# Kernel optimization log

Hardware: AMD Instinct MI355X
Metric: run time of the kernel (lower is better)

Reference implementation:

```python
import jax, jax.numpy as jnp
import numpy as np

B, S, D = 4, 4096, 2048
DFF = 4 * D
SKIP = 0.125


def setup_inputs() -> dict:
    key = jax.random.key(0)
    ks = jax.random.split(key, 4)
    s_in = 1.0 / np.sqrt(D).astype(np.float32)
    s_ff = 1.0 / np.sqrt(DFF).astype(np.float32)
    return {
        "x": jax.random.normal(ks[0], (B, S, D), jnp.float32),
        "Wr": jax.random.normal(ks[1], (D, 1), jnp.float32) * s_in,
        "br": jnp.zeros((1,), jnp.float32),
        "W1": jax.random.normal(ks[2], (D, DFF), jnp.float32) * s_in,
        "b1": jnp.zeros((DFF,), jnp.float32),
        "W2": jax.random.normal(ks[3], (DFF, D), jnp.float32) * s_ff,
        "b2": jnp.zeros((D,), jnp.float32),
    }


def reference(x, Wr, br, W1, b1, W2, b2):
    Bs, Ss, Ds = x.shape
    k = max(int(Ss * SKIP), 1)
    # Router: tiny linear D -> 1
    logits = (x @ Wr + br)[..., 0]                      # [B, S]
    # Top-k token selection along sequence
    weights, idx = jax.lax.top_k(logits, k)             # [B, k] (unsorted order within topk)
    perm = jnp.argsort(idx, axis=1)                     # torch.sort's sort-indices
    tokens = jnp.take_along_axis(idx, perm, axis=1)     # sorted token positions [B, k]
    # Gather selected tokens
    fx = jnp.take_along_axis(x, tokens[..., None], axis=1)  # [B, k, D]
    h = jax.nn.gelu(fx @ W1 + b1, approximate=False)    # [B, k, 4D]
    out_l = h @ W2 + b2                                  # [B, k, D]
    # Softmax over topk router logits, reordered to sorted-token order
    tw = jax.nn.softmax(weights, axis=1)                # [B, k]
    rw = jnp.take_along_axis(tw, perm, axis=1)          # [B, k]
    xw = rw[..., None] * out_l                           # [B, k, D]
    # scatter_add back onto x at the selected token positions
    bidx = jnp.arange(Bs)[:, None]                       # [B, 1]
    return x.at[bidx, tokens].add(xw)
```

## Files before the change

### kernel.cpp

```cpp
#include <hip/hip_runtime.h>
#include <math.h>

#define B_DIM   4
#define S_DIM   4096
#define D_DIM   2048
#define DFF_DIM 8192
#define K_TOP   512
#define M_ROWS  (B_DIM * K_TOP)
#define NSPLIT  4

typedef _Float16 half8 __attribute__((ext_vector_type(8)));
typedef _Float16 half4 __attribute__((ext_vector_type(4)));
typedef float    floatx4 __attribute__((ext_vector_type(4)));

static const size_t OFF_LOGITS = 0;
static const size_t OFF_SELMAP = 0;
static const size_t OFF_TOK    = 65536;
static const size_t OFF_RW     = 73728;
static const size_t OFF_FX     = 81920;
static const size_t OFF_W1T    = OFF_FX  + (size_t)M_ROWS * D_DIM * 2;
static const size_t OFF_W2T    = OFF_W1T + (size_t)DFF_DIM * D_DIM * 2;
static const size_t OFF_H      = OFF_W2T + (size_t)D_DIM * DFF_DIM * 2;
static const size_t WS_NEEDED  = OFF_H   + (size_t)M_ROWS * DFF_DIM * 2;
static const size_t OFF_PART   = OFF_W1T;

__device__ __forceinline__ void async_ld16(const void* g, void* l) {
  __builtin_amdgcn_global_load_lds((const __attribute__((address_space(1))) unsigned int*)g,
                                   (__attribute__((address_space(3))) unsigned int*)l,
                                   16, 0, 0);
}

#define WAITCNT_VM4   0x0F74
#define WAITCNT_VM0   0x0F70
#define WAITCNT_LGKM0 0xC07F

__global__ __launch_bounds__(256) void router_logits(const float* __restrict__ x,
                                                     const float* __restrict__ Wr,
                                                     const float* __restrict__ br,
                                                     float* __restrict__ logits) {
  int row  = blockIdx.x * 4 + (threadIdx.x >> 6);
  int lane = threadIdx.x & 63;
  const float4* xr = (const float4*)(x + (size_t)row * D_DIM);
  const float4* wr = (const float4*)Wr;
  float s = 0.f;
#pragma unroll
  for (int i = 0; i < (D_DIM / 4) / 64; ++i) {
    float4 a = xr[lane + i * 64];
    float4 w = wr[lane + i * 64];
    s += a.x * w.x + a.y * w.y + a.z * w.z + a.w * w.w;
  }
#pragma unroll
  for (int off = 32; off > 0; off >>= 1) s += __shfl_down(s, off, 64);
  if (lane == 0) logits[row] = s + br[0];
}

__global__ __launch_bounds__(256) void topk_select(const float* logits,
                                                   int* selmap,
                                                   int* __restrict__ tokens,
                                                   float* __restrict__ rw) {
  int b = blockIdx.x;
  const float* lg = logits + (size_t)b * S_DIM;
  __shared__ unsigned int keys[S_DIM];
  __shared__ unsigned int bins[256];
  __shared__ unsigned int sscan[256];
  __shared__ unsigned int sh_prefix, sh_r;
  __shared__ float sel_logit[K_TOP];
  __shared__ float red[8];

  int tid = threadIdx.x;
  for (int s = tid; s < S_DIM; s += 256) {
    unsigned int u = __float_as_uint(lg[s]);
    keys[s] = (u & 0x80000000u) ? ~u : (u | 0x80000000u);
    selmap[b * S_DIM + s] = -1;
  }
  if (tid == 0) { sh_prefix = 0u; sh_r = K_TOP; }
  __syncthreads();

  for (int p = 24; p >= 0; p -= 8) {
    bins[tid] = 0u;
    __syncthreads();
    unsigned int prefix = sh_prefix;
    unsigned int maskhi = (p == 24) ? 0u : (0xFFFFFFFFu << (p + 8));
    for (int s = tid; s < S_DIM; s += 256) {
      unsigned int kk = keys[s];
      if ((kk & maskhi) == prefix) atomicAdd(&bins[(kk >> p) & 255u], 1u);
    }
    __syncthreads();
    sscan[tid] = bins[255 - tid];
    __syncthreads();
#pragma unroll
    for (int off = 1; off < 256; off <<= 1) {
      unsigned int v = (tid >= off) ? sscan[tid - off] : 0u;
      __syncthreads();
      sscan[tid] += v;
      __syncthreads();
    }
    unsigned int r = sh_r;
    unsigned int above = (tid > 0) ? sscan[tid - 1] : 0u;
    bool hit = (sscan[tid] >= r) && (above < r);
    __syncthreads();
    if (hit) {
      sh_prefix = prefix | ((unsigned int)(255 - tid) << p);
      sh_r = r - above;
    }
    __syncthreads();
  }
  unsigned int T = sh_prefix;

  int s0 = tid * 16;
  unsigned int g = 0, e = 0;
#pragma unroll
  for (int j = 0; j < 16; ++j) {
    unsigned int kk = keys[s0 + j];
    g += (kk > T);
    e += (kk == T);
  }
  sscan[tid] = g | (e << 16);
  __syncthreads();
#pragma unroll
  for (int off = 1; off < 256; off <<= 1) {
    unsigned int v = (tid >= off) ? sscan[tid - off] : 0u;
    __syncthreads();
    sscan[tid] += v;
    __syncthreads();
  }
  unsigned int incl = sscan[tid];
  unsigned int Gtot = sscan[255] & 0xFFFFu;
  unsigned int need = (unsigned int)K_TOP - Gtot;
  unsigned int gr = (incl & 0xFFFFu) - g;
  unsigned int er = (incl >> 16) - e;
#pragma unroll
  for (int j = 0; j < 16; ++j) {
    unsigned int kk = keys[s0 + j];
    if (kk > T) {
      unsigned int pos = gr + (er < need ? er : need);
      tokens[b * K_TOP + (int)pos] = s0 + j;
      sel_logit[pos] = __uint_as_float((kk & 0x80000000u) ? (kk & 0x7FFFFFFFu) : ~kk);
      selmap[b * S_DIM + s0 + j] = (int)pos;
      gr++;
    } else if (kk == T) {
      if (er < need) {
        unsigned int pos = gr + er;
        tokens[b * K_TOP + (int)pos] = s0 + j;
        sel_logit[pos] = __uint_as_float((kk & 0x80000000u) ? (kk & 0x7FFFFFFFu) : ~kk);
        selmap[b * S_DIM + s0 + j] = (int)pos;
      }
      er++;
    }
  }
  __syncthreads();

  int lane = tid & 63, wv = tid >> 6;
  float mx = -1e30f;
  for (int i = tid; i < K_TOP; i += 256) mx = fmaxf(mx, sel_logit[i]);
#pragma unroll
  for (int off = 32; off > 0; off >>= 1) mx = fmaxf(mx, __shfl_down(mx, off, 64));
  if (lane == 0) red[wv] = mx;
  __syncthreads();
  if (tid == 0) red[0] = fmaxf(fmaxf(red[0], red[1]), fmaxf(red[2], red[3]));
  __syncthreads();
  float M = red[0];
  float sm = 0.f;
  for (int i = tid; i < K_TOP; i += 256) sm += expf(sel_logit[i] - M);
#pragma unroll
  for (int off = 32; off > 0; off >>= 1) sm += __shfl_down(sm, off, 64);
  if (lane == 0) red[4 + wv] = sm;
  __syncthreads();
  if (tid == 0) red[4] = red[4] + red[5] + red[6] + red[7];
  __syncthreads();
  float SUM = red[4];
  for (int i = tid; i < K_TOP; i += 256) rw[b * K_TOP + i] = expf(sel_logit[i] - M) / SUM;
}

__global__ __launch_bounds__(256) void transpose_cvt(const float* __restrict__ in,
                                                     _Float16* __restrict__ out,
                                                     int K, int N) {
  __shared__ float tile[64][65];
  int nb = blockIdx.x * 64, kb = blockIdx.y * 64;
  int tid = threadIdx.x;
  int lr = tid >> 4;
  int lc = (tid & 15) * 4;
#pragma unroll
  for (int p = 0; p < 4; ++p) {
    int row = p * 16 + lr;
    float4 v = *(const float4*)(in + (size_t)(kb + row) * N + nb + lc);
    tile[row][lc] = v.x; tile[row][lc + 1] = v.y; tile[row][lc + 2] = v.z; tile[row][lc + 3] = v.w;
  }
  __syncthreads();
#pragma unroll
  for (int p = 0; p < 2; ++p) {
    int cc = p * 256 + tid;
    int n  = cc >> 3;
    int kc = (cc & 7) * 8;
    half8 o;
#pragma unroll
    for (int j = 0; j < 8; ++j) o[j] = (_Float16)tile[kc + j][n];
    *(half8*)(out + (size_t)(nb + n) * K + kb + kc) = o;
  }
}

__global__ __launch_bounds__(256) void gather_cvt(const float* __restrict__ x,
                                                  const int* __restrict__ tokens,
                                                  _Float16* __restrict__ fx) {
  int row = blockIdx.x;
  int b = row >> 9;
  int token = tokens[row];
  const float4* src = (const float4*)(x + ((size_t)b * S_DIM + token) * D_DIM);
  half4* dst = (half4*)(fx + (size_t)row * D_DIM);
  for (int i = threadIdx.x; i < D_DIM / 4; i += 256) {
    float4 v = src[i];
    half4 o;
    o[0] = (_Float16)v.x; o[1] = (_Float16)v.y; o[2] = (_Float16)v.z; o[3] = (_Float16)v.w;
    dst[i] = o;
  }
}

template <int EPI>
__global__ __launch_bounds__(256) void gemm_bt(const _Float16* __restrict__ A,
                                               const _Float16* __restrict__ Bt,
                                               const float* __restrict__ bias,
                                               _Float16* __restrict__ Co,
                                               int M, int N, int K, int Kspan) {
  __shared__ _Float16 As[2][128 * 32];
  __shared__ _Float16 Bs[2][128 * 32];
  const int tid = threadIdx.x;
  const int lane = tid & 63;
  const int wave = tid >> 6;
  const int bm = blockIdx.y * 128;
  const int bn = blockIdx.x * 128;
  const int wm = (wave & 1) * 64;
  const int wn = (wave >> 1) * 64;
  const int mr = lane & 15;
  const int sw = ((lane >> 4) ^ ((lane >> 1) & 3)) * 8;
  const int k0 = blockIdx.z * Kspan;
  const int kend = k0 + Kspan;

  const int c0 = (wave * 2) * 64 + lane;
  const int c1 = (wave * 2 + 1) * 64 + lane;
  const int m0 = c0 >> 2, g0 = (c0 & 3) ^ ((m0 >> 1) & 3);
  const int m1 = c1 >> 2, g1 = (c1 & 3) ^ ((m1 >> 1) & 3);
  const _Float16* a0p = A  + (size_t)(bm + m0) * K + g0 * 8;
  const _Float16* a1p = A  + (size_t)(bm + m1) * K + g1 * 8;
  const _Float16* b0p = Bt + (size_t)(bn + m0) * K + g0 * 8;
  const _Float16* b1p = Bt + (size_t)(bn + m1) * K + g1 * 8;
  const int slot0 = (wave * 2) * 512;
  const int slot1 = (wave * 2 + 1) * 512;

  floatx4 acc[4][4] = {};

  async_ld16(a0p + k0, &As[0][slot0]);
  async_ld16(b0p + k0, &Bs[0][slot0]);
  async_ld16(a1p + k0, &As[0][slot1]);
  async_ld16(b1p + k0, &Bs[0][slot1]);

  for (int kt = k0; kt < kend; kt += 64) {
    {
      int kn = kt + 32;
      async_ld16(a0p + kn, &As[1][slot0]);
      async_ld16(b0p + kn, &Bs[1][slot0]);
      async_ld16(a1p + kn, &As[1][slot1]);
      async_ld16(b1p + kn, &Bs[1][slot1]);
      __builtin_amdgcn_s_waitcnt(WAITCNT_VM4);
    }
    __builtin_amdgcn_s_barrier();
    {
      half8 af[4], bf[4];
#pragma unroll
      for (int i = 0; i < 4; ++i) af[i] = *(const half8*)(&As[0][(wm + i * 16 + mr) * 32 + sw]);
#pragma unroll
      for (int j = 0; j < 4; ++j) bf[j] = *(const half8*)(&Bs[0][(wn + j * 16 + mr) * 32 + sw]);
#pragma unroll
      for (int i = 0; i < 4; ++i)
#pragma unroll
        for (int j = 0; j < 4; ++j)
          acc[i][j] = __builtin_amdgcn_mfma_f32_16x16x32_f16(af[i], bf[j], acc[i][j], 0, 0, 0);
    }
    __builtin_amdgcn_s_waitcnt(WAITCNT_LGKM0);
    __builtin_amdgcn_s_barrier();

    if (kt + 64 < kend) {
      int kn = kt + 64;
      async_ld16(a0p + kn, &As[0][slot0]);
      async_ld16(b0p + kn, &Bs[0][slot0]);
      async_ld16(a1p + kn, &As[0][slot1]);
      async_ld16(b1p + kn, &Bs[0][slot1]);
      __builtin_amdgcn_s_waitcnt(WAITCNT_VM4);
    } else {
      __builtin_amdgcn_s_waitcnt(WAITCNT_VM0);
    }
    __builtin_amdgcn_s_barrier();
    {
      half8 af[4], bf[4];
#pragma unroll
      for (int i = 0; i < 4; ++i) af[i] = *(const half8*)(&As[1][(wm + i * 16 + mr) * 32 + sw]);
#pragma unroll
      for (int j = 0; j < 4; ++j) bf[j] = *(const half8*)(&Bs[1][(wn + j * 16 + mr) * 32 + sw]);
#pragma unroll
      for (int i = 0; i < 4; ++i)
#pragma unroll
        for (int j = 0; j < 4; ++j)
          acc[i][j] = __builtin_amdgcn_mfma_f32_16x16x32_f16(af[i], bf[j], acc[i][j], 0, 0, 0);
    }
    __builtin_amdgcn_s_waitcnt(WAITCNT_LGKM0);
    __builtin_amdgcn_s_barrier();
  }

  const int r0 = (lane >> 4) * 4;
  const int cn = lane & 15;
  if (EPI == 0) {
#pragma unroll
    for (int i = 0; i < 4; ++i)
#pragma unroll
      for (int j = 0; j < 4; ++j) {
        int col = bn + wn + j * 16 + cn;
        float bv = bias[col];
#pragma unroll
        for (int r = 0; r < 4; ++r) {
          int row = bm + wm + i * 16 + r0 + r;
          float v = acc[i][j][r] + bv;
          v = 0.5f * v * (1.0f + erff(v * 0.7071067811865475f));
          Co[(size_t)row * N + col] = (_Float16)v;
        }
      }
  } else {
    size_t zoff = (size_t)blockIdx.z * M;
#pragma unroll
    for (int i = 0; i < 4; ++i)
#pragma unroll
      for (int j = 0; j < 4; ++j) {
        int col = bn + wn + j * 16 + cn;
#pragma unroll
        for (int r = 0; r < 4; ++r) {
          int row = bm + wm + i * 16 + r0 + r;
          Co[(zoff + row) * N + col] = (_Float16)acc[i][j][r];
        }
      }
  }
}

__global__ __launch_bounds__(256) void finalize(const float* __restrict__ x,
                                                const _Float16* __restrict__ part,
                                                const float* __restrict__ bias,
                                                const int* __restrict__ selmap,
                                                const float* __restrict__ rw,
                                                float* __restrict__ out) {
  int row = blockIdx.x;
  size_t base = (size_t)row * D_DIM;
  int sel = selmap[row];
  int c = threadIdx.x * 8;
  float4 o0 = *(const float4*)(x + base + c);
  float4 o1 = *(const float4*)(x + base + c + 4);
  if (sel >= 0) {
    float wgt = rw[sel];
    float acc[8] = {0, 0, 0, 0, 0, 0, 0, 0};
#pragma unroll
    for (int kz = 0; kz < NSPLIT; ++kz) {
      half8 p = *(const half8*)(part + ((size_t)kz * M_ROWS + sel) * D_DIM + c);
#pragma unroll
      for (int j = 0; j < 8; ++j) acc[j] += (float)p[j];
    }
    float4 b0 = *(const float4*)(bias + c);
    float4 b1 = *(const float4*)(bias + c + 4);
    o0.x += wgt * (acc[0] + b0.x);
    o0.y += wgt * (acc[1] + b0.y);
    o0.z += wgt * (acc[2] + b0.z);
    o0.w += wgt * (acc[3] + b0.w);
    o1.x += wgt * (acc[4] + b1.x);
    o1.y += wgt * (acc[5] + b1.y);
    o1.z += wgt * (acc[6] + b1.z);
    o1.w += wgt * (acc[7] + b1.w);
  }
  *(float4*)(out + base + c)     = o0;
  *(float4*)(out + base + c + 4) = o1;
}

extern "C" void kernel_launch(void* const* d_in, const int* in_sizes, int n_in,
                              void* d_out, int out_size, void* d_ws, size_t ws_size,
                              hipStream_t stream) {
  const float* x  = (const float*)d_in[0];
  const float* Wr = (const float*)d_in[1];
  const float* br = (const float*)d_in[2];
  const float* W1 = (const float*)d_in[3];
  const float* b1 = (const float*)d_in[4];
  const float* W2 = (const float*)d_in[5];
  const float* b2 = (const float*)d_in[6];
  float* out = (float*)d_out;

  if (ws_size < WS_NEEDED) return;

  char* ws = (char*)d_ws;
  float*     logits = (float*)(ws + OFF_LOGITS);
  int*       selmap = (int*)(ws + OFF_SELMAP);
  int*       tokens = (int*)(ws + OFF_TOK);
  float*     rw     = (float*)(ws + OFF_RW);
  _Float16*  fx     = (_Float16*)(ws + OFF_FX);
  _Float16*  W1T    = (_Float16*)(ws + OFF_W1T);
  _Float16*  W2T    = (_Float16*)(ws + OFF_W2T);
  _Float16*  h      = (_Float16*)(ws + OFF_H);
  _Float16*  part   = (_Float16*)(ws + OFF_PART);

  transpose_cvt<<<dim3(DFF_DIM / 64, D_DIM / 64), 256, 0, stream>>>(W1, W1T, D_DIM, DFF_DIM);
  transpose_cvt<<<dim3(D_DIM / 64, DFF_DIM / 64), 256, 0, stream>>>(W2, W2T, DFF_DIM, D_DIM);

  router_logits<<<(B_DIM * S_DIM) / 4, 256, 0, stream>>>(x, Wr, br, logits);
  topk_select<<<B_DIM, 256, 0, stream>>>(logits, selmap, tokens, rw);
  gather_cvt<<<M_ROWS, 256, 0, stream>>>(x, tokens, fx);

  gemm_bt<0><<<dim3(DFF_DIM / 128, M_ROWS / 128, 1), 256, 0, stream>>>(
      fx, W1T, b1, h, M_ROWS, DFF_DIM, D_DIM, D_DIM);
  gemm_bt<2><<<dim3(D_DIM / 128, M_ROWS / 128, NSPLIT), 256, 0, stream>>>(
      h, W2T, nullptr, part, M_ROWS, D_DIM, DFF_DIM, DFF_DIM / NSPLIT);
  finalize<<<B_DIM * S_DIM, 256, 0, stream>>>(x, part, b2, selmap, rw, out);
}
```

Measured before the change: 600.7 us.

## Replace 128x128 GEMM with 256x256 tile, 8-wave kernel and block swizzle

Both FFN GEMMs move to a new kernel with 256x256 output tiles, 512 threads (8 waves) and 64-wide K tiles in double-buffered LDS. The K loop runs in four MFMA phases with s_setprio around the math, an XOR swizzle on the LDS layout, and a workgroup remap that groups blocks for L2 reuse. The aim is more reuse per loaded byte and more MFMA work per barrier. In exchange the kernel needs 128 KB of LDS per block and many more accumulator registers, and the second GEMM runs fewer blocks (8x8x4), which can limit occupancy.

```diff
diff --git a/kernel.cpp b/kernel.cpp
--- a/kernel.cpp
+++ b/kernel.cpp
@@ -30,7 +30,6 @@
                                    16, 0, 0);
 }
 
-#define WAITCNT_VM4   0x0F74
 #define WAITCNT_VM0   0x0F70
 #define WAITCNT_LGKM0 0xC07F
 
@@ -216,92 +215,135 @@
 }
 
 template <int EPI>
-__global__ __launch_bounds__(256) void gemm_bt(const _Float16* __restrict__ A,
-                                               const _Float16* __restrict__ Bt,
-                                               const float* __restrict__ bias,
-                                               _Float16* __restrict__ Co,
-                                               int M, int N, int K, int Kspan) {
-  __shared__ _Float16 As[2][128 * 32];
-  __shared__ _Float16 Bs[2][128 * 32];
-  const int tid = threadIdx.x;
+__global__ __launch_bounds__(512, 2) void gemm256(const _Float16* __restrict__ A,
+                                                  const _Float16* __restrict__ Bt,
+                                                  const float* __restrict__ bias,
+                                                  _Float16* __restrict__ Co,
+                                                  int M, int N, int K, int Kspan) {
+  __shared__ _Float16 As[2][256 * 64];
+  __shared__ _Float16 Bs[2][256 * 64];
+  const int tid  = threadIdx.x;
   const int lane = tid & 63;
   const int wave = tid >> 6;
-  const int bm = blockIdx.y * 128;
-  const int bn = blockIdx.x * 128;
-  const int wm = (wave & 1) * 64;
-  const int wn = (wave >> 1) * 64;
-  const int mr = lane & 15;
-  const int sw = ((lane >> 4) ^ ((lane >> 1) & 3)) * 8;
+  const int wm   = wave >> 2;
+  const int wn   = wave & 3;
+
+  const int nwg = gridDim.x * gridDim.y;
+  const int bid = blockIdx.y * gridDim.x + blockIdx.x;
+  const int swb = (bid & 7) * (nwg >> 3) + (bid >> 3);
+  const int bn  = (swb % gridDim.x) * 256;
+  const int bm  = (swb / gridDim.x) * 256;
+
   const int k0 = blockIdx.z * Kspan;
-  const int kend = k0 + Kspan;
-
-  const int c0 = (wave * 2) * 64 + lane;
-  const int c1 = (wave * 2 + 1) * 64 + lane;
-  const int m0 = c0 >> 2, g0 = (c0 & 3) ^ ((m0 >> 1) & 3);
-  const int m1 = c1 >> 2, g1 = (c1 & 3) ^ ((m1 >> 1) & 3);
-  const _Float16* a0p = A  + (size_t)(bm + m0) * K + g0 * 8;
-  const _Float16* a1p = A  + (size_t)(bm + m1) * K + g1 * 8;
-  const _Float16* b0p = Bt + (size_t)(bn + m0) * K + g0 * 8;
-  const _Float16* b1p = Bt + (size_t)(bn + m1) * K + g1 * 8;
-  const int slot0 = (wave * 2) * 512;
-  const int slot1 = (wave * 2 + 1) * 512;
-
-  floatx4 acc[4][4] = {};
-
-  async_ld16(a0p + k0, &As[0][slot0]);
-  async_ld16(b0p + k0, &Bs[0][slot0]);
-  async_ld16(a1p + k0, &As[0][slot1]);
-  async_ld16(b1p + k0, &Bs[0][slot1]);
-
-  for (int kt = k0; kt < kend; kt += 64) {
-    {
-      int kn = kt + 32;
-      async_ld16(a0p + kn, &As[1][slot0]);
-      async_ld16(b0p + kn, &Bs[1][slot0]);
-      async_ld16(a1p + kn, &As[1][slot1]);
-      async_ld16(b1p + kn, &Bs[1][slot1]);
-      __builtin_amdgcn_s_waitcnt(WAITCNT_VM4);
-    }
-    __builtin_amdgcn_s_barrier();
-    {
-      half8 af[4], bf[4];
-#pragma unroll
-      for (int i = 0; i < 4; ++i) af[i] = *(const half8*)(&As[0][(wm + i * 16 + mr) * 32 + sw]);
-#pragma unroll
-      for (int j = 0; j < 4; ++j) bf[j] = *(const half8*)(&Bs[0][(wn + j * 16 + mr) * 32 + sw]);
-#pragma unroll
-      for (int i = 0; i < 4; ++i)
-#pragma unroll
-        for (int j = 0; j < 4; ++j)
-          acc[i][j] = __builtin_amdgcn_mfma_f32_16x16x32_f16(af[i], bf[j], acc[i][j], 0, 0, 0);
-    }
+  const int nt = Kspan / 64;
+
+  const int lr  = lane >> 3;
+  const int lcs = ((lane & 7) ^ lr) * 8;
+  const _Float16* sa[2][2];
+  const _Float16* sb[2][2];
+  int ldso[2][2];
+#pragma unroll
+  for (int h = 0; h < 2; ++h)
+#pragma unroll
+    for (int ci = 0; ci < 2; ++ci) {
+      const int cip = 2 * wave + ci;
+      const int r   = h * 128 + cip * 8 + lr;
+      sa[h][ci] = A  + (size_t)(bm + r) * K + k0 + lcs;
+      sb[h][ci] = Bt + (size_t)(bn + r) * K + k0 + lcs;
+      ldso[h][ci] = h * 8192 + cip * 512;
+    }
+
+  const int mr   = lane & 15;
+  const int ksub = lane >> 4;
+  const int xr   = mr & 7;
+  const int sc0  = (ksub ^ xr) * 8;
+  const int sc1  = ((ksub ^ xr) ^ 4) * 8;
+  const int aro  = (wm * 128 + mr) * 64;
+  const int bro  = (wn * 64 + mr) * 64;
+
+  floatx4 acc[8][4] = {};
+
+#pragma unroll
+  for (int h = 0; h < 2; ++h)
+#pragma unroll
+    for (int ci = 0; ci < 2; ++ci) {
+      async_ld16(sa[h][ci], &As[0][ldso[h][ci]]);
+      async_ld16(sb[h][ci], &Bs[0][ldso[h][ci]]);
+    }
+  __builtin_amdgcn_s_waitcnt(WAITCNT_VM0);
+  __builtin_amdgcn_s_barrier();
+
+  for (int t = 0; t < nt; ++t) {
+    const _Float16* as = As[t & 1];
+    const _Float16* bs = Bs[t & 1];
+    half8 af[4], bf[4];
+
+#pragma unroll
+    for (int i = 0; i < 4; ++i) af[i] = *(const half8*)(as + aro + i * 1024 + sc0);
+#pragma unroll
+    for (int j = 0; j < 4; ++j) bf[j] = *(const half8*)(bs + bro + j * 1024 + sc0);
+    if (t + 1 < nt) {
+      const int nb = (t + 1) & 1;
+      const int kt = (t + 1) * 64;
+#pragma unroll
+      for (int h = 0; h < 2; ++h)
+#pragma unroll
+        for (int ci = 0; ci < 2; ++ci) {
+          async_ld16(sa[h][ci] + kt, &As[nb][ldso[h][ci]]);
+          async_ld16(sb[h][ci] + kt, &Bs[nb][ldso[h][ci]]);
+        }
+    }
+    __builtin_amdgcn_s_barrier();
     __builtin_amdgcn_s_waitcnt(WAITCNT_LGKM0);
-    __builtin_amdgcn_s_barrier();
-
-    if (kt + 64 < kend) {
-      int kn = kt + 64;
-      async_ld16(a0p + kn, &As[0][slot0]);
-      async_ld16(b0p + kn, &Bs[0][slot0]);
-      async_ld16(a1p + kn, &As[0][slot1]);
-      async_ld16(b1p + kn, &Bs[0][slot1]);
-      __builtin_amdgcn_s_waitcnt(WAITCNT_VM4);
-    } else {
-      __builtin_amdgcn_s_waitcnt(WAITCNT_VM0);
-    }
-    __builtin_amdgcn_s_barrier();
-    {
-      half8 af[4], bf[4];
-#pragma unroll
-      for (int i = 0; i < 4; ++i) af[i] = *(const half8*)(&As[1][(wm + i * 16 + mr) * 32 + sw]);
-#pragma unroll
-      for (int j = 0; j < 4; ++j) bf[j] = *(const half8*)(&Bs[1][(wn + j * 16 + mr) * 32 + sw]);
-#pragma unroll
-      for (int i = 0; i < 4; ++i)
-#pragma unroll
-        for (int j = 0; j < 4; ++j)
-          acc[i][j] = __builtin_amdgcn_mfma_f32_16x16x32_f16(af[i], bf[j], acc[i][j], 0, 0, 0);
-    }
+    __builtin_amdgcn_s_setprio(1);
+#pragma unroll
+    for (int i = 0; i < 4; ++i)
+#pragma unroll
+      for (int j = 0; j < 4; ++j)
+        acc[i][j] = __builtin_amdgcn_mfma_f32_16x16x32_f16(af[i], bf[j], acc[i][j], 0, 0, 0);
+    __builtin_amdgcn_s_setprio(0);
+    __builtin_amdgcn_s_barrier();
+
+#pragma unroll
+    for (int i = 0; i < 4; ++i) af[i] = *(const half8*)(as + aro + 4096 + i * 1024 + sc0);
+    __builtin_amdgcn_s_barrier();
     __builtin_amdgcn_s_waitcnt(WAITCNT_LGKM0);
+    __builtin_amdgcn_s_setprio(1);
+#pragma unroll
+    for (int i = 0; i < 4; ++i)
+#pragma unroll
+      for (int j = 0; j < 4; ++j)
+        acc[4 + i][j] = __builtin_amdgcn_mfma_f32_16x16x32_f16(af[i], bf[j], acc[4 + i][j], 0, 0, 0);
+    __builtin_amdgcn_s_setprio(0);
+    __builtin_amdgcn_s_barrier();
+
+#pragma unroll
+    for (int i = 0; i < 4; ++i) af[i] = *(const half8*)(as + aro + i * 1024 + sc1);
+#pragma unroll
+    for (int j = 0; j < 4; ++j) bf[j] = *(const half8*)(bs + bro + j * 1024 + sc1);
+    __builtin_amdgcn_s_barrier();
+    __builtin_amdgcn_s_waitcnt(WAITCNT_LGKM0);
+    __builtin_amdgcn_s_setprio(1);
+#pragma unroll
+    for (int i = 0; i < 4; ++i)
+#pragma unroll
+      for (int j = 0; j < 4; ++j)
+        acc[i][j] = __builtin_amdgcn_mfma_f32_16x16x32_f16(af[i], bf[j], acc[i][j], 0, 0, 0);
+    __builtin_amdgcn_s_setprio(0);
+    __builtin_amdgcn_s_barrier();
+
+#pragma unroll
+    for (int i = 0; i < 4; ++i) af[i] = *(const half8*)(as + aro + 4096 + i * 1024 + sc1);
+    __builtin_amdgcn_s_barrier();
+    __builtin_amdgcn_s_waitcnt(WAITCNT_LGKM0);
+    __builtin_amdgcn_s_setprio(1);
+#pragma unroll
+    for (int i = 0; i < 4; ++i)
+#pragma unroll
+      for (int j = 0; j < 4; ++j)
+        acc[4 + i][j] = __builtin_amdgcn_mfma_f32_16x16x32_f16(af[i], bf[j], acc[4 + i][j], 0, 0, 0);
+    __builtin_amdgcn_s_setprio(0);
+    __builtin_amdgcn_s_waitcnt(WAITCNT_VM0);
     __builtin_amdgcn_s_barrier();
   }
 
@@ -309,32 +351,33 @@
   const int cn = lane & 15;
   if (EPI == 0) {
 #pragma unroll
-    for (int i = 0; i < 4; ++i)
+    for (int i = 0; i < 8; ++i) {
+      const int row = bm + wm * 128 + (i >> 2) * 64 + (i & 3) * 16 + r0;
 #pragma unroll
       for (int j = 0; j < 4; ++j) {
-        int col = bn + wn + j * 16 + cn;
-        float bv = bias[col];
+        const int col = bn + wn * 64 + j * 16 + cn;
+        const float bv = bias[col];
 #pragma unroll
         for (int r = 0; r < 4; ++r) {
-          int row = bm + wm + i * 16 + r0 + r;
           float v = acc[i][j][r] + bv;
           v = 0.5f * v * (1.0f + erff(v * 0.7071067811865475f));
-          Co[(size_t)row * N + col] = (_Float16)v;
+          Co[(size_t)(row + r) * N + col] = (_Float16)v;
         }
       }
+    }
   } else {
-    size_t zoff = (size_t)blockIdx.z * M;
-#pragma unroll
-    for (int i = 0; i < 4; ++i)
+    const size_t zoff = (size_t)blockIdx.z * M;
+#pragma unroll
+    for (int i = 0; i < 8; ++i) {
+      const int row = bm + wm * 128 + (i >> 2) * 64 + (i & 3) * 16 + r0;
 #pragma unroll
       for (int j = 0; j < 4; ++j) {
-        int col = bn + wn + j * 16 + cn;
-#pragma unroll
-        for (int r = 0; r < 4; ++r) {
-          int row = bm + wm + i * 16 + r0 + r;
-          Co[(zoff + row) * N + col] = (_Float16)acc[i][j][r];
-        }
+        const int col = bn + wn * 64 + j * 16 + cn;
+#pragma unroll
+        for (int r = 0; r < 4; ++r)
+          Co[(zoff + row + r) * N + col] = (_Float16)acc[i][j][r];
       }
+    }
   }
 }
 
@@ -406,9 +449,9 @@
   topk_select<<<B_DIM, 256, 0, stream>>>(logits, selmap, tokens, rw);
   gather_cvt<<<M_ROWS, 256, 0, stream>>>(x, tokens, fx);
 
-  gemm_bt<0><<<dim3(DFF_DIM / 128, M_ROWS / 128, 1), 256, 0, stream>>>(
+  gemm256<0><<<dim3(DFF_DIM / 256, M_ROWS / 256, 1), 512, 0, stream>>>(
       fx, W1T, b1, h, M_ROWS, DFF_DIM, D_DIM, D_DIM);
-  gemm_bt<2><<<dim3(D_DIM / 128, M_ROWS / 128, NSPLIT), 256, 0, stream>>>(
+  gemm256<2><<<dim3(D_DIM / 256, M_ROWS / 256, NSPLIT), 512, 0, stream>>>(
       h, W2T, nullptr, part, M_ROWS, D_DIM, DFF_DIM, DFF_DIM / NSPLIT);
   finalize<<<B_DIM * S_DIM, 256, 0, stream>>>(x, part, b2, selmap, rw, out);
 }
```

Measured after the change: 570.0 us. 1.05x faster.
